# Performance work log

Hardware: AMD Instinct MI355X
Metric: run time of the kernel (lower is better)

The kernel has to match this reference:

```python
import jax, jax.numpy as jnp
import numpy as np

NG, NT, E = 2500, 20000, 640000
SRC_DIM, DST_DIM, HID, OUT, NCLS = 128, 500, 128, 128, 16


def setup_inputs() -> dict:
    key = jax.random.key(0)
    ks = jax.random.split(key, 11)
    d = {
        "gene_feats": jax.random.normal(ks[0], (NG, SRC_DIM), jnp.float32),
        "train_feats": jax.random.normal(ks[1], (NT, DST_DIM), jnp.float32),
        "edge_src": jax.random.randint(ks[2], (E,), 0, NG),
        "edge_dst": jax.random.randint(ks[3], (E,), 0, NT),
        # conv1: SAGEConv((src_dim, dst_dim) -> hidden)
        "W1_neigh": jax.random.normal(ks[4], (SRC_DIM, HID), jnp.float32) / np.sqrt(SRC_DIM),
        "W1_self": jax.random.normal(ks[5], (DST_DIM, HID), jnp.float32) / np.sqrt(DST_DIM),
        "b1": jnp.zeros((HID,), jnp.float32),
        # conv2: SAGEConv(hidden -> out); src input is the raw gene features
        "W2_neigh": jax.random.normal(ks[6], (HID, OUT), jnp.float32) / np.sqrt(HID),
        "W2_self": jax.random.normal(ks[7], (HID, OUT), jnp.float32) / np.sqrt(HID),
        "b2": jnp.zeros((OUT,), jnp.float32),
        # classifier MLP
        "Wc1": jax.random.normal(ks[8], (OUT, OUT), jnp.float32) / np.sqrt(OUT),
        "bc1": jnp.zeros((OUT,), jnp.float32),
        "Wc2": jax.random.normal(ks[9], (OUT, NCLS), jnp.float32) / np.sqrt(OUT),
        "bc2": jnp.zeros((NCLS,), jnp.float32),
    }
    return d


def _segment_mean(msgs, dst, num_segments):
    # mean over in-edges; isolated dst nodes get 0 (DGL convention)
    sums = jax.ops.segment_sum(msgs, dst, num_segments=num_segments)
    cnt = jax.ops.segment_sum(jnp.ones((msgs.shape[0],), msgs.dtype), dst,
                              num_segments=num_segments)
    return sums / jnp.maximum(cnt, 1.0)[:, None]


def reference(gene_feats, train_feats, edge_src, edge_dst,
              W1_neigh, W1_self, b1, W2_neigh, W2_self, b2,
              Wc1, bc1, Wc2, bc2):
    # mean-aggregate gene (src) features onto train (dst) nodes
    agg = _segment_mean(gene_feats[edge_src], edge_dst, NT)  # [NT, SRC_DIM]
    # conv1: fc_self(h_dst) + fc_neigh(mean_neigh) + bias, then ReLU
    h1 = jax.nn.relu(train_feats @ W1_self + agg @ W1_neigh + b1)  # [NT, HID]
    # conv2 reuses raw gene features as src -> same mean aggregation
    h2 = jax.nn.relu(h1 @ W2_self + agg @ W2_neigh + b2)  # [NT, OUT]
    # classifier: Linear -> ReLU -> Linear
    return jax.nn.relu(h2 @ Wc1 + bc1) @ Wc2 + bc2  # [NT, NCLS]
```

## Files before the change

### kernel.cpp

```cpp
#include <hip/hip_runtime.h>


#define NG 2500
#define NT 20000
#define NE 640000
#define NCLS 16
#define CAP 96
#define BCAP 1536
#define NBIN 625

typedef unsigned short u16;
typedef unsigned int u32;

typedef float f32x4 __attribute__((ext_vector_type(4)));
typedef __bf16 bf16x8 __attribute__((ext_vector_type(8)));

__device__ __forceinline__ float b2f(u16 u) { return __uint_as_float(((u32)u) << 16); }
__device__ __forceinline__ float blo(u32 p) { return __uint_as_float(p << 16); }
__device__ __forceinline__ float bhi(u32 p) { return __uint_as_float(p & 0xffff0000u); }
__device__ __forceinline__ u16 f2b(float f) {
    u32 u = __float_as_uint(f);
    return (u16)((u + 0x7fffu + ((u >> 16) & 1u)) >> 16);
}

#define B1N 81920
#define B2N 32768
#define B3N 16384
#define B4N 2048
#define NEB 625
#define GNB 625
#define PKB 520

__global__ __launch_bounds__(256) void k_prep(
    const int* __restrict__ edst,
    u32* __restrict__ hist,
    const float* __restrict__ gene, u32* __restrict__ GH32,
    const float* __restrict__ W1n, const float* __restrict__ W1s,
    const float* __restrict__ W2n, const float* __restrict__ W2s,
    const float* __restrict__ Wc1, const float* __restrict__ Wc2,
    u16* __restrict__ B1h, u16* __restrict__ B1l,
    u16* __restrict__ B2h, u16* __restrict__ B2l,
    u16* __restrict__ B3h, u16* __restrict__ B3l,
    u16* __restrict__ B4h, u16* __restrict__ B4l) {
    int blk = blockIdx.x, t = threadIdx.x;
    if (blk < NEB) {
        __shared__ u32 lh[NBIN];
        for (int i = t; i < NBIN; i += 256) lh[i] = 0;
        __syncthreads();
        int e0 = (blk * 256 + t) * 4;
        const int4 d4 = *(const int4*)(edst + e0);
        int dd[4] = {d4.x, d4.y, d4.z, d4.w};
#pragma unroll
        for (int i = 0; i < 4; ++i) {
            unsigned d = (unsigned)dd[i];
            if (d < NT) atomicAdd(&lh[d >> 5], 1u);
        }
        __syncthreads();
        for (int i = t; i < NBIN; i += 256)
            hist[(size_t)blk * NBIN + i] = lh[i];
        return;
    }
    if (blk < NEB + GNB) {
        int idx = (blk - NEB) * 256 + t;
        float2 v = ((const float2*)gene)[idx];
        GH32[idx] = (u32)f2b(v.x) | ((u32)f2b(v.y) << 16);
        return;
    }
    int idx = (blk - NEB - GNB) * 256 + t;
    float v = 0.f;
    u16 *ph = 0, *pl = 0;
    int off = 0;
    if (idx < B1N) {
        int j = idx & 7, l = (idx >> 3) & 63, rest = idx >> 9;
        int g = rest & 7, kk = rest >> 3;
        int k = kk * 32 + ((l >> 4) << 3) + j, n = (g << 4) + (l & 15);
        if (k < 500) v = W1s[k * 128 + n];
        else if (k >= 512) v = W1n[(k - 512) * 128 + n];
        ph = B1h; pl = B1l; off = idx;
    } else if (idx < B1N + B2N) {
        int e = idx - B1N;
        int j = e & 7, l = (e >> 3) & 63, rest = e >> 9;
        int g = rest & 7, kk = rest >> 3;
        int k = kk * 32 + ((l >> 4) << 3) + j, n = (g << 4) + (l & 15);
        v = (k < 128) ? W2s[k * 128 + n] : W2n[(k - 128) * 128 + n];
        ph = B2h; pl = B2l; off = e;
    } else if (idx < B1N + B2N + B3N) {
        int e = idx - (B1N + B2N);
        int j = e & 7, l = (e >> 3) & 63, rest = e >> 9;
        int g = rest & 7, kk = rest >> 3;
        int k = kk * 32 + ((l >> 4) << 3) + j, n = (g << 4) + (l & 15);
        v = Wc1[k * 128 + n];
        ph = B3h; pl = B3l; off = e;
    } else if (idx < B1N + B2N + B3N + B4N) {
        int e = idx - (B1N + B2N + B3N);
        int j = e & 7, l = (e >> 3) & 63, kk = e >> 9;
        int k = kk * 32 + ((l >> 4) << 3) + j, n = l & 15;
        v = Wc2[k * 16 + n];
        ph = B4h; pl = B4l; off = e;
    }
    if (ph) {
        u16 hi = f2b(v);
        u16 lo = f2b(v - b2f(hi));
        ph[off] = hi;
        pl[off] = lo;
    }
}

__global__ __launch_bounds__(256) void k_scan(
    const u32* __restrict__ hist, u32* __restrict__ boff,
    int* __restrict__ bcnt) {
    int bin = blockIdx.x, t = threadIdx.x;
    __shared__ u32 part[256];
    u32 s0 = 0, s1 = 0, s2 = 0;
    int i0 = 3 * t;
    if (i0 < NBIN) s0 = hist[(size_t)i0 * NBIN + bin];
    if (i0 + 1 < NBIN) s1 = hist[(size_t)(i0 + 1) * NBIN + bin];
    if (i0 + 2 < NBIN) s2 = hist[(size_t)(i0 + 2) * NBIN + bin];
    u32 mine = s0 + s1 + s2;
    part[t] = mine;
    __syncthreads();
    for (int off = 1; off < 256; off <<= 1) {
        u32 x = (t >= off) ? part[t - off] : 0u;
        __syncthreads();
        part[t] += x;
        __syncthreads();
    }
    u32 base = part[t] - mine;
    if (i0 < NBIN) boff[(size_t)bin * NBIN + i0] = base;
    if (i0 + 1 < NBIN) boff[(size_t)bin * NBIN + i0 + 1] = base + s0;
    if (i0 + 2 < NBIN) boff[(size_t)bin * NBIN + i0 + 2] = base + s0 + s1;
    if (t == 255) bcnt[bin] = (int)part[255];
}

__global__ __launch_bounds__(256) void k_scat(
    const int* __restrict__ esrc, const int* __restrict__ edst,
    const u32* __restrict__ boff, u32* __restrict__ bkt) {
    int blk = blockIdx.x, t = threadIdx.x;
    __shared__ u32 lcur[NBIN];
    for (int i = t; i < NBIN; i += 256) lcur[i] = 0;
    __syncthreads();
    int e0 = (blk * 256 + t) * 4;
    const int4 s4 = *(const int4*)(esrc + e0);
    const int4 d4 = *(const int4*)(edst + e0);
    int ss[4] = {s4.x, s4.y, s4.z, s4.w};
    int dd[4] = {d4.x, d4.y, d4.z, d4.w};
#pragma unroll
    for (int i = 0; i < 4; ++i) {
        unsigned d = (unsigned)dd[i];
        if (d < NT) {
            int bin = (int)(d >> 5);
            u32 rank = atomicAdd(&lcur[bin], 1u);
            u32 pos = boff[(size_t)bin * NBIN + blk] + rank;
            if (pos < BCAP)
                bkt[(size_t)bin * BCAP + pos] = ((d & 31u) << 16) | (u32)ss[i];
        }
    }
}

__global__ __launch_bounds__(256, 8) void k_agg(
    const int* __restrict__ bcnt, const u32* __restrict__ bkt,
    const u16* __restrict__ GH,
    u32* __restrict__ AGH, u32* __restrict__ AGL) {
    __shared__ __align__(16) u16 SRT[16 * CAP];
    __shared__ int POS[16];
    int t = threadIdx.x;
    int bk = blockIdx.x >> 1, half = blockIdx.x & 1;

    if (t < 16) POS[t] = 0;
    int bc = bcnt[bk];
    if (bc > BCAP) bc = BCAP;
    __syncthreads();

    int rlo = half * 16;
    for (int i = t; i < bc; i += 256) {
        u32 e = bkt[(size_t)bk * BCAP + i];
        int r = (int)(e >> 16) - rlo;
        if ((unsigned)r < 16u) {
            int p = atomicAdd(&POS[r], 1);
            if (p < CAP) SRT[r * CAP + p] = (u16)(e & 0xffffu);
        }
    }
    __syncthreads();

    int gr = t >> 4, cg = t & 15;
    int ctrue = POS[gr];
    int c = ctrue > CAP ? CAP : ctrue;
    const u16* crow = SRT + gr * CAP;
    int nfull = c >> 3;
    uint4 i40 = *(const uint4*)(crow);
    uint4 i41 = *(const uint4*)(crow + 8);
    uint4 i42 = *(const uint4*)(crow + 16);
    uint4 i43 = *(const uint4*)(crow + 24);
    float a[8];
#pragma unroll
    for (int p = 0; p < 8; ++p) a[p] = 0.f;

#define ACC(p)                                      \
    do {                                            \
        a[0] += blo((p).x); a[1] += bhi((p).x);     \
        a[2] += blo((p).y); a[3] += bhi((p).y);     \
        a[4] += blo((p).z); a[5] += bhi((p).z);     \
        a[6] += blo((p).w); a[7] += bhi((p).w);     \
    } while (0)
    auto GHLoad = [&](int s) -> uint4 {
        return *(const uint4*)(GH + (size_t)s * 128 + cg * 8);
    };
    auto batch8 = [&](uint4 iq) {
        uint4 P0 = GHLoad((int)(iq.x & 0xffffu));
        uint4 P1 = GHLoad((int)(iq.x >> 16));
        uint4 P2 = GHLoad((int)(iq.y & 0xffffu));
        uint4 P3 = GHLoad((int)(iq.y >> 16));
        uint4 P4 = GHLoad((int)(iq.z & 0xffffu));
        uint4 P5 = GHLoad((int)(iq.z >> 16));
        uint4 P6 = GHLoad((int)(iq.w & 0xffffu));
        uint4 P7 = GHLoad((int)(iq.w >> 16));
        ACC(P0); ACC(P1); ACC(P2); ACC(P3);
        ACC(P4); ACC(P5); ACC(P6); ACC(P7);
    };

    if (nfull > 0) batch8(i40);
    if (nfull > 1) batch8(i41);
    if (nfull > 2) batch8(i42);
    if (nfull > 3) batch8(i43);
    for (int b = 4; b < nfull; ++b) batch8(*(const uint4*)(crow + b * 8));
    {
        int j = nfull * 8;
        if (j < c) {
            uint4 i4 = *(const uint4*)(crow + j);
            u32 w[4] = {i4.x, i4.y, i4.z, i4.w};
#pragma unroll
            for (int k = 0; k < 8; ++k) {
                int s = (int)((w[k >> 1] >> ((k & 1) * 16)) & 0xffffu);
                bool live = (j + k) < c;
                s = live ? s : 0;
                uint4 p = GHLoad(s);
                if (live) ACC(p);
            }
        }
    }
#undef ACC

    float inv = (ctrue > 0) ? 1.f / (float)ctrue : 0.f;
    size_t base = (size_t)(blockIdx.x * 16 + gr) * 64 + cg * 4;
#pragma unroll
    for (int p = 0; p < 4; ++p) {
        float x = a[2 * p] * inv, y = a[2 * p + 1] * inv;
        u16 hx = f2b(x), hy = f2b(y);
        AGH[base + p] = (u32)hx | ((u32)hy << 16);
        AGL[base + p] = (u32)f2b(x - b2f(hx)) | ((u32)f2b(y - b2f(hy)) << 16);
    }
}

__global__ __launch_bounds__(512, 4) void k_mlp(
    const u32* __restrict__ AGH, const u32* __restrict__ AGL,
    const float* __restrict__ train,
    const u16* __restrict__ B1h, const u16* __restrict__ B1l,
    const u16* __restrict__ B2h, const u16* __restrict__ B2l,
    const u16* __restrict__ B3h, const u16* __restrict__ B3l,
    const u16* __restrict__ B4h, const u16* __restrict__ B4l,
    const float* __restrict__ b1, const float* __restrict__ b2,
    const float* __restrict__ bc1, const float* __restrict__ bc2,
    float* __restrict__ out) {
    __shared__ __align__(16) u16 SMEM[26112];
    u16* SAGh = SMEM;
    u16* SAGl = SMEM + 4352;
    u16* S1h = SMEM + 8704;
    u16* S1l = SMEM + 13056;
    u16* S2h = SMEM + 17408;
    u16* S2l = SMEM + 21760;
    u16* TS = SMEM + 8704;

    int t = threadIdx.x;
    int row0 = blockIdx.x * 32;

    float4 st[8];
    {
        const float4* tb = (const float4*)(train + (size_t)row0 * 500);
#pragma unroll
        for (int i = 0; i < 7; ++i) st[i] = tb[t + i * 512];
        if (t < 416) st[7] = tb[t + 3584];
    }
    uint4 ah4 = ((const uint4*)AGH)[(size_t)row0 * 16 + t];
    uint4 al4 = ((const uint4*)AGL)[(size_t)row0 * 16 + t];

    {
        u32* T32 = (u32*)TS;
#pragma unroll
        for (int i = 0; i < 8; ++i) {
            int idx = t + i * 512;
            if (i == 7 && t >= 416) break;
            int r = idx / 125, c4 = idx - r * 125;
            int base = r * 260 + c4 * 2;
            T32[base] = (u32)f2b(st[i].x) | ((u32)f2b(st[i].y) << 16);
            T32[base + 1] = (u32)f2b(st[i].z) | ((u32)f2b(st[i].w) << 16);
        }
        if (t < 192) {
            int r = t / 6, c4 = t - r * 6;
            T32[r * 260 + 250 + c4] = 0;
        }
    }
    {
        int r = t >> 4, c16 = t & 15;
        int base = r * 68 + c16 * 4;
        u32* SH = (u32*)SAGh;
        u32* SL = (u32*)SAGl;
        SH[base] = ah4.x; SH[base + 1] = ah4.y;
        SH[base + 2] = ah4.z; SH[base + 3] = ah4.w;
        SL[base] = al4.x; SL[base + 1] = al4.y;
        SL[base + 2] = al4.z; SL[base + 3] = al4.w;
    }
    __syncthreads();

    int lane = t & 63, g = t >> 6;
    int m = lane & 15, q = lane >> 4, n16 = lane & 15;

    int hr0 = m * 136 + q * 8;
    int hr1 = (16 + m) * 136 + q * 8;
    int cr0 = q * 4, cr1 = 16 + q * 4;
    const f32x4 z4 = {0.f, 0.f, 0.f, 0.f};
    f32x4 acc0 = z4, acc1 = z4;
    const u16* tA0 = TS + m * 520 + q * 8;
    const u16* tA1 = TS + (16 + m) * 520 + q * 8;

#pragma unroll
    for (int kk = 0; kk < 16; ++kk) {
        bf16x8 a0 = *(const bf16x8*)(tA0 + kk * 32);
        bf16x8 a1 = *(const bf16x8*)(tA1 + kk * 32);
        size_t bo = ((size_t)(kk * 8 + g) * 64 + lane) * 8;
        bf16x8 bh = *(const bf16x8*)(B1h + bo);
        bf16x8 bl = *(const bf16x8*)(B1l + bo);
        acc0 = __builtin_amdgcn_mfma_f32_16x16x32_bf16(a0, bh, acc0, 0, 0, 0);
        acc0 = __builtin_amdgcn_mfma_f32_16x16x32_bf16(a0, bl, acc0, 0, 0, 0);
        acc1 = __builtin_amdgcn_mfma_f32_16x16x32_bf16(a1, bh, acc1, 0, 0, 0);
        acc1 = __builtin_amdgcn_mfma_f32_16x16x32_bf16(a1, bl, acc1, 0, 0, 0);
    }
#pragma unroll
    for (int kk = 16; kk < 20; ++kk) {
        int o = (kk - 16) * 32;
        bf16x8 ah0 = *(const bf16x8*)(SAGh + hr0 + o);
        bf16x8 al0 = *(const bf16x8*)(SAGl + hr0 + o);
        bf16x8 ah1 = *(const bf16x8*)(SAGh + hr1 + o);
        bf16x8 al1 = *(const bf16x8*)(SAGl + hr1 + o);
        size_t bo = ((size_t)(kk * 8 + g) * 64 + lane) * 8;
        bf16x8 bh = *(const bf16x8*)(B1h + bo);
        bf16x8 bl = *(const bf16x8*)(B1l + bo);
        acc0 = __builtin_amdgcn_mfma_f32_16x16x32_bf16(ah0, bh, acc0, 0, 0, 0);
        acc0 = __builtin_amdgcn_mfma_f32_16x16x32_bf16(ah0, bl, acc0, 0, 0, 0);
        acc0 = __builtin_amdgcn_mfma_f32_16x16x32_bf16(al0, bh, acc0, 0, 0, 0);
        acc1 = __builtin_amdgcn_mfma_f32_16x16x32_bf16(ah1, bh, acc1, 0, 0, 0);
        acc1 = __builtin_amdgcn_mfma_f32_16x16x32_bf16(ah1, bl, acc1, 0, 0, 0);
        acc1 = __builtin_amdgcn_mfma_f32_16x16x32_bf16(al1, bh, acc1, 0, 0, 0);
    }
    __syncthreads();
    {
        int n = g * 16 + n16;
        float bias = b1[n];
#pragma unroll
        for (int rg = 0; rg < 4; ++rg) {
            float v0 = acc0[rg] + bias; v0 = v0 > 0.f ? v0 : 0.f;
            float v1 = acc1[rg] + bias; v1 = v1 > 0.f ? v1 : 0.f;
            u16 h0 = f2b(v0), h1v = f2b(v1);
            S1h[(cr0 + rg) * 136 + n] = h0; S1l[(cr0 + rg) * 136 + n] = f2b(v0 - b2f(h0));
            S1h[(cr1 + rg) * 136 + n] = h1v; S1l[(cr1 + rg) * 136 + n] = f2b(v1 - b2f(h1v));
        }
    }
    __syncthreads();

    acc0 = z4; acc1 = z4;
#pragma unroll
    for (int kk = 0; kk < 8; ++kk) {
        const u16* Ph = (kk < 4) ? S1h : SAGh;
        const u16* Pl = (kk < 4) ? S1l : SAGl;
        int o = (kk & 3) * 32;
        bf16x8 ah0 = *(const bf16x8*)(Ph + hr0 + o);
        bf16x8 al0 = *(const bf16x8*)(Pl + hr0 + o);
        bf16x8 ah1 = *(const bf16x8*)(Ph + hr1 + o);
        bf16x8 al1 = *(const bf16x8*)(Pl + hr1 + o);
        size_t bo = ((size_t)(kk * 8 + g) * 64 + lane) * 8;
        bf16x8 bh = *(const bf16x8*)(B2h + bo);
        bf16x8 bl = *(const bf16x8*)(B2l + bo);
        acc0 = __builtin_amdgcn_mfma_f32_16x16x32_bf16(ah0, bh, acc0, 0, 0, 0);
        acc0 = __builtin_amdgcn_mfma_f32_16x16x32_bf16(ah0, bl, acc0, 0, 0, 0);
        acc0 = __builtin_amdgcn_mfma_f32_16x16x32_bf16(al0, bh, acc0, 0, 0, 0);
        acc1 = __builtin_amdgcn_mfma_f32_16x16x32_bf16(ah1, bh, acc1, 0, 0, 0);
        acc1 = __builtin_amdgcn_mfma_f32_16x16x32_bf16(ah1, bl, acc1, 0, 0, 0);
        acc1 = __builtin_amdgcn_mfma_f32_16x16x32_bf16(al1, bh, acc1, 0, 0, 0);
    }
    {
        int n = g * 16 + n16;
        float bias = b2[n];
#pragma unroll
        for (int rg = 0; rg < 4; ++rg) {
            float v0 = acc0[rg] + bias; v0 = v0 > 0.f ? v0 : 0.f;
            float v1 = acc1[rg] + bias; v1 = v1 > 0.f ? v1 : 0.f;
            u16 h0 = f2b(v0), h1v = f2b(v1);
            S2h[(cr0 + rg) * 136 + n] = h0; S2l[(cr0 + rg) * 136 + n] = f2b(v0 - b2f(h0));
            S2h[(cr1 + rg) * 136 + n] = h1v; S2l[(cr1 + rg) * 136 + n] = f2b(v1 - b2f(h1v));
        }
    }
    __syncthreads();

    acc0 = z4; acc1 = z4;
#pragma unroll
    for (int kk = 0; kk < 4; ++kk) {
        int o = kk * 32;
        bf16x8 ah0 = *(const bf16x8*)(S2h + hr0 + o);
        bf16x8 al0 = *(const bf16x8*)(S2l + hr0 + o);
        bf16x8 ah1 = *(const bf16x8*)(S2h + hr1 + o);
        bf16x8 al1 = *(const bf16x8*)(S2l + hr1 + o);
        size_t bo = ((size_t)(kk * 8 + g) * 64 + lane) * 8;
        bf16x8 bh = *(const bf16x8*)(B3h + bo);
        bf16x8 bl = *(const bf16x8*)(B3l + bo);
        acc0 = __builtin_amdgcn_mfma_f32_16x16x32_bf16(ah0, bh, acc0, 0, 0, 0);
        acc0 = __builtin_amdgcn_mfma_f32_16x16x32_bf16(ah0, bl, acc0, 0, 0, 0);
        acc0 = __builtin_amdgcn_mfma_f32_16x16x32_bf16(al0, bh, acc0, 0, 0, 0);
        acc1 = __builtin_amdgcn_mfma_f32_16x16x32_bf16(ah1, bh, acc1, 0, 0, 0);
        acc1 = __builtin_amdgcn_mfma_f32_16x16x32_bf16(ah1, bl, acc1, 0, 0, 0);
        acc1 = __builtin_amdgcn_mfma_f32_16x16x32_bf16(al1, bh, acc1, 0, 0, 0);
    }
    {
        int n = g * 16 + n16;
        float bias = bc1[n];
#pragma unroll
        for (int rg = 0; rg < 4; ++rg) {
            float v0 = acc0[rg] + bias; v0 = v0 > 0.f ? v0 : 0.f;
            float v1 = acc1[rg] + bias; v1 = v1 > 0.f ? v1 : 0.f;
            u16 h0 = f2b(v0), h1v = f2b(v1);
            S1h[(cr0 + rg) * 136 + n] = h0; S1l[(cr0 + rg) * 136 + n] = f2b(v0 - b2f(h0));
            S1h[(cr1 + rg) * 136 + n] = h1v; S1l[(cr1 + rg) * 136 + n] = f2b(v1 - b2f(h1v));
        }
    }
    __syncthreads();

    if (g < 2) {
        int hr = (g == 0) ? hr0 : hr1;
        int cr = (g == 0) ? cr0 : cr1;
        f32x4 a4 = z4;
#pragma unroll
        for (int kk = 0; kk < 4; ++kk) {
            bf16x8 ah = *(const bf16x8*)(S1h + hr + kk * 32);
            bf16x8 al = *(const bf16x8*)(S1l + hr + kk * 32);
            size_t bo = ((size_t)kk * 64 + lane) * 8;
            bf16x8 bh = *(const bf16x8*)(B4h + bo);
            bf16x8 bl = *(const bf16x8*)(B4l + bo);
            a4 = __builtin_amdgcn_mfma_f32_16x16x32_bf16(ah, bh, a4, 0, 0, 0);
            a4 = __builtin_amdgcn_mfma_f32_16x16x32_bf16(ah, bl, a4, 0, 0, 0);
            a4 = __builtin_amdgcn_mfma_f32_16x16x32_bf16(al, bh, a4, 0, 0, 0);
        }
        float bias = bc2[n16];
#pragma unroll
        for (int rg = 0; rg < 4; ++rg)
            out[(size_t)(row0 + cr + rg) * NCLS + n16] = a4[rg] + bias;
    }
}

extern "C" void kernel_launch(void* const* d_in, const int* in_sizes, int n_in,
                              void* d_out, int out_size, void* d_ws, size_t ws_size,
                              hipStream_t stream) {
    const float* gene = (const float*)d_in[0];
    const float* train = (const float*)d_in[1];
    const int* esrc = (const int*)d_in[2];
    const int* edst = (const int*)d_in[3];

    char* ws = (char*)d_ws;
    int* bcnt = (int*)(ws + 0);
    u32* hist = (u32*)(ws + 4096);
    u32* boff = (u32*)(ws + 1566720);
    u32* bkt = (u32*)(ws + 3129344);
    u16* GH = (u16*)(ws + 6969344);
    u32* AGH = (u32*)(ws + 7609344);
    u32* AGL = (u32*)(ws + 12729344);
    u16* B1h = (u16*)(ws + 17849344);
    u16* B1l = (u16*)(ws + 18013184);
    u16* B2h = (u16*)(ws + 18177024);
    u16* B2l = (u16*)(ws + 18242560);
    u16* B3h = (u16*)(ws + 18308096);
    u16* B3l = (u16*)(ws + 18340864);
    u16* B4h = (u16*)(ws + 18373632);
    u16* B4l = (u16*)(ws + 18377728);

    k_prep<<<NEB + GNB + PKB, 256, 0, stream>>>(
        edst, hist, gene, (u32*)GH,
        (const float*)d_in[4], (const float*)d_in[5], (const float*)d_in[7],
        (const float*)d_in[8], (const float*)d_in[10], (const float*)d_in[12],
        B1h, B1l, B2h, B2l, B3h, B3l, B4h, B4l);
    k_scan<<<NBIN, 256, 0, stream>>>(hist, boff, bcnt);
    k_scat<<<NEB, 256, 0, stream>>>(esrc, edst, boff, bkt);
    k_agg<<<NT / 16, 256, 0, stream>>>(bcnt, bkt, GH, AGH, AGL);
    k_mlp<<<NT / 32, 512, 0, stream>>>(
        AGH, AGL, train, B1h, B1l, B2h, B2l, B3h, B3l, B4h, B4l,
        (const float*)d_in[6], (const float*)d_in[9], (const float*)d_in[11],
        (const float*)d_in[13], (float*)d_out);
}
```

Measured before the change: 153.8 us.

## Fuse prep, scan, scatter and aggregation into one cooperative kernel with grid syncs

```diff
diff --git a/kernel.cpp b/kernel.cpp
--- a/kernel.cpp
+++ b/kernel.cpp
@@ -1,4 +1,7 @@
 #include <hip/hip_runtime.h>
+#include <hip/hip_cooperative_groups.h>
+
+namespace cg = cooperative_groups;
 
 
 #define NG 2500
@@ -30,43 +33,13 @@
 #define NEB 625
 #define GNB 625
 #define PKB 520
-
-__global__ __launch_bounds__(256) void k_prep(
-    const int* __restrict__ edst,
-    u32* __restrict__ hist,
-    const float* __restrict__ gene, u32* __restrict__ GH32,
-    const float* __restrict__ W1n, const float* __restrict__ W1s,
-    const float* __restrict__ W2n, const float* __restrict__ W2s,
-    const float* __restrict__ Wc1, const float* __restrict__ Wc2,
-    u16* __restrict__ B1h, u16* __restrict__ B1l,
-    u16* __restrict__ B2h, u16* __restrict__ B2l,
-    u16* __restrict__ B3h, u16* __restrict__ B3l,
-    u16* __restrict__ B4h, u16* __restrict__ B4l) {
-    int blk = blockIdx.x, t = threadIdx.x;
-    if (blk < NEB) {
-        __shared__ u32 lh[NBIN];
-        for (int i = t; i < NBIN; i += 256) lh[i] = 0;
-        __syncthreads();
-        int e0 = (blk * 256 + t) * 4;
-        const int4 d4 = *(const int4*)(edst + e0);
-        int dd[4] = {d4.x, d4.y, d4.z, d4.w};
-#pragma unroll
-        for (int i = 0; i < 4; ++i) {
-            unsigned d = (unsigned)dd[i];
-            if (d < NT) atomicAdd(&lh[d >> 5], 1u);
-        }
-        __syncthreads();
-        for (int i = t; i < NBIN; i += 256)
-            hist[(size_t)blk * NBIN + i] = lh[i];
-        return;
-    }
-    if (blk < NEB + GNB) {
-        int idx = (blk - NEB) * 256 + t;
-        float2 v = ((const float2*)gene)[idx];
-        GH32[idx] = (u32)f2b(v.x) | ((u32)f2b(v.y) << 16);
-        return;
-    }
-    int idx = (blk - NEB - GNB) * 256 + t;
+#define NCB (NEB + GNB + PKB)
+
+__device__ __forceinline__ void pack_one(
+    int idx, const float* W1n, const float* W1s, const float* W2n,
+    const float* W2s, const float* Wc1, const float* Wc2,
+    u16* B1h, u16* B1l, u16* B2h, u16* B2l, u16* B3h, u16* B3l,
+    u16* B4h, u16* B4l) {
     float v = 0.f;
     u16 *ph = 0, *pl = 0;
     int off = 0;
@@ -106,66 +79,10 @@
     }
 }
 
-__global__ __launch_bounds__(256) void k_scan(
-    const u32* __restrict__ hist, u32* __restrict__ boff,
-    int* __restrict__ bcnt) {
-    int bin = blockIdx.x, t = threadIdx.x;
-    __shared__ u32 part[256];
-    u32 s0 = 0, s1 = 0, s2 = 0;
-    int i0 = 3 * t;
-    if (i0 < NBIN) s0 = hist[(size_t)i0 * NBIN + bin];
-    if (i0 + 1 < NBIN) s1 = hist[(size_t)(i0 + 1) * NBIN + bin];
-    if (i0 + 2 < NBIN) s2 = hist[(size_t)(i0 + 2) * NBIN + bin];
-    u32 mine = s0 + s1 + s2;
-    part[t] = mine;
-    __syncthreads();
-    for (int off = 1; off < 256; off <<= 1) {
-        u32 x = (t >= off) ? part[t - off] : 0u;
-        __syncthreads();
-        part[t] += x;
-        __syncthreads();
-    }
-    u32 base = part[t] - mine;
-    if (i0 < NBIN) boff[(size_t)bin * NBIN + i0] = base;
-    if (i0 + 1 < NBIN) boff[(size_t)bin * NBIN + i0 + 1] = base + s0;
-    if (i0 + 2 < NBIN) boff[(size_t)bin * NBIN + i0 + 2] = base + s0 + s1;
-    if (t == 255) bcnt[bin] = (int)part[255];
-}
-
-__global__ __launch_bounds__(256) void k_scat(
-    const int* __restrict__ esrc, const int* __restrict__ edst,
-    const u32* __restrict__ boff, u32* __restrict__ bkt) {
-    int blk = blockIdx.x, t = threadIdx.x;
-    __shared__ u32 lcur[NBIN];
-    for (int i = t; i < NBIN; i += 256) lcur[i] = 0;
-    __syncthreads();
-    int e0 = (blk * 256 + t) * 4;
-    const int4 s4 = *(const int4*)(esrc + e0);
-    const int4 d4 = *(const int4*)(edst + e0);
-    int ss[4] = {s4.x, s4.y, s4.z, s4.w};
-    int dd[4] = {d4.x, d4.y, d4.z, d4.w};
-#pragma unroll
-    for (int i = 0; i < 4; ++i) {
-        unsigned d = (unsigned)dd[i];
-        if (d < NT) {
-            int bin = (int)(d >> 5);
-            u32 rank = atomicAdd(&lcur[bin], 1u);
-            u32 pos = boff[(size_t)bin * NBIN + blk] + rank;
-            if (pos < BCAP)
-                bkt[(size_t)bin * BCAP + pos] = ((d & 31u) << 16) | (u32)ss[i];
-        }
-    }
-}
-
-__global__ __launch_bounds__(256, 8) void k_agg(
-    const int* __restrict__ bcnt, const u32* __restrict__ bkt,
-    const u16* __restrict__ GH,
-    u32* __restrict__ AGH, u32* __restrict__ AGL) {
-    __shared__ __align__(16) u16 SRT[16 * CAP];
-    __shared__ int POS[16];
-    int t = threadIdx.x;
-    int bk = blockIdx.x >> 1, half = blockIdx.x & 1;
-
+__device__ __forceinline__ void agg_body(
+    int blk16, const int* bcnt, const u32* bkt, const u16* GH,
+    u32* AGH, u32* AGL, u16* SRT, int* POS, int t) {
+    int bk = blk16 >> 1, half = blk16 & 1;
     if (t < 16) POS[t] = 0;
     int bc = bcnt[bk];
     if (bc > BCAP) bc = BCAP;
@@ -182,7 +99,7 @@
     }
     __syncthreads();
 
-    int gr = t >> 4, cg = t & 15;
+    int gr = t >> 4, cg16 = t & 15;
     int ctrue = POS[gr];
     int c = ctrue > CAP ? CAP : ctrue;
     const u16* crow = SRT + gr * CAP;
@@ -203,7 +120,7 @@
         a[6] += blo((p).w); a[7] += bhi((p).w);     \
     } while (0)
     auto GHLoad = [&](int s) -> uint4 {
-        return *(const uint4*)(GH + (size_t)s * 128 + cg * 8);
+        return *(const uint4*)(GH + (size_t)s * 128 + cg16 * 8);
     };
     auto batch8 = [&](uint4 iq) {
         uint4 P0 = GHLoad((int)(iq.x & 0xffffu));
@@ -241,7 +158,7 @@
 #undef ACC
 
     float inv = (ctrue > 0) ? 1.f / (float)ctrue : 0.f;
-    size_t base = (size_t)(blockIdx.x * 16 + gr) * 64 + cg * 4;
+    size_t base = (size_t)(blk16 * 16 + gr) * 64 + cg16 * 4;
 #pragma unroll
     for (int p = 0; p < 4; ++p) {
         float x = a[2 * p] * inv, y = a[2 * p + 1] * inv;
@@ -249,6 +166,205 @@
         AGH[base + p] = (u32)hx | ((u32)hy << 16);
         AGL[base + p] = (u32)f2b(x - b2f(hx)) | ((u32)f2b(y - b2f(hy)) << 16);
     }
+}
+
+__global__ __launch_bounds__(256, 8) void k_coop(
+    const int* __restrict__ esrc, const int* __restrict__ edst,
+    u32* __restrict__ hist, u32* __restrict__ boff, int* __restrict__ bcnt,
+    u32* __restrict__ bkt,
+    const float* __restrict__ gene, u32* __restrict__ GH32,
+    const u16* __restrict__ GH,
+    u32* __restrict__ AGH, u32* __restrict__ AGL,
+    const float* __restrict__ W1n, const float* __restrict__ W1s,
+    const float* __restrict__ W2n, const float* __restrict__ W2s,
+    const float* __restrict__ Wc1, const float* __restrict__ Wc2,
+    u16* __restrict__ B1h, u16* __restrict__ B1l,
+    u16* __restrict__ B2h, u16* __restrict__ B2l,
+    u16* __restrict__ B3h, u16* __restrict__ B3l,
+    u16* __restrict__ B4h, u16* __restrict__ B4l) {
+    __shared__ __align__(16) u32 UN[800];
+    u32* lh = UN;
+    u32* part = UN;
+    u32* lcur = UN;
+    u16* SRT = (u16*)UN;
+    int* POS = (int*)(UN + 768);
+
+    cg::grid_group grid = cg::this_grid();
+    int blk = blockIdx.x, t = threadIdx.x;
+
+    int4 s4 = {0, 0, 0, 0}, d4 = {0, 0, 0, 0};
+
+    if (blk < NEB) {
+        for (int i = t; i < NBIN; i += 256) lh[i] = 0;
+        __syncthreads();
+        int e0 = (blk * 256 + t) * 4;
+        s4 = *(const int4*)(esrc + e0);
+        d4 = *(const int4*)(edst + e0);
+        int dd[4] = {d4.x, d4.y, d4.z, d4.w};
+#pragma unroll
+        for (int i = 0; i < 4; ++i) {
+            unsigned d = (unsigned)dd[i];
+            if (d < NT) atomicAdd(&lh[d >> 5], 1u);
+        }
+        __syncthreads();
+        for (int i = t; i < NBIN; i += 256)
+            hist[(size_t)blk * NBIN + i] = lh[i];
+    } else if (blk < NEB + GNB) {
+        int idx = (blk - NEB) * 256 + t;
+        float2 v = ((const float2*)gene)[idx];
+        GH32[idx] = (u32)f2b(v.x) | ((u32)f2b(v.y) << 16);
+    } else {
+        int idx = (blk - NEB - GNB) * 256 + t;
+        pack_one(idx, W1n, W1s, W2n, W2s, Wc1, Wc2,
+                 B1h, B1l, B2h, B2l, B3h, B3l, B4h, B4l);
+    }
+    grid.sync();
+
+    if (blk < NBIN) {
+        int bin = blk;
+        u32 s0 = 0, s1 = 0, s2 = 0;
+        int i0 = 3 * t;
+        if (i0 < NBIN) s0 = hist[(size_t)i0 * NBIN + bin];
+        if (i0 + 1 < NBIN) s1 = hist[(size_t)(i0 + 1) * NBIN + bin];
+        if (i0 + 2 < NBIN) s2 = hist[(size_t)(i0 + 2) * NBIN + bin];
+        u32 mine = s0 + s1 + s2;
+        part[t] = mine;
+        __syncthreads();
+        for (int off = 1; off < 256; off <<= 1) {
+            u32 x = (t >= off) ? part[t - off] : 0u;
+            __syncthreads();
+            part[t] += x;
+            __syncthreads();
+        }
+        u32 base = part[t] - mine;
+        if (i0 < NBIN) boff[(size_t)bin * NBIN + i0] = base;
+        if (i0 + 1 < NBIN) boff[(size_t)bin * NBIN + i0 + 1] = base + s0;
+        if (i0 + 2 < NBIN) boff[(size_t)bin * NBIN + i0 + 2] = base + s0 + s1;
+        if (t == 255) bcnt[bin] = (int)part[255];
+    }
+    grid.sync();
+
+    if (blk < NEB) {
+        for (int i = t; i < NBIN; i += 256) lcur[i] = 0;
+        __syncthreads();
+        int ss[4] = {s4.x, s4.y, s4.z, s4.w};
+        int dd[4] = {d4.x, d4.y, d4.z, d4.w};
+#pragma unroll
+        for (int i = 0; i < 4; ++i) {
+            unsigned d = (unsigned)dd[i];
+            if (d < NT) {
+                int bin = (int)(d >> 5);
+                u32 rank = atomicAdd(&lcur[bin], 1u);
+                u32 pos = boff[(size_t)bin * NBIN + blk] + rank;
+                if (pos < BCAP)
+                    bkt[(size_t)bin * BCAP + pos] =
+                        ((d & 31u) << 16) | (u32)ss[i];
+            }
+        }
+    }
+    grid.sync();
+
+    if (blk < NT / 16)
+        agg_body(blk, bcnt, bkt, GH, AGH, AGL, SRT, POS, t);
+}
+
+__global__ __launch_bounds__(256) void k_prep(
+    const int* __restrict__ edst,
+    u32* __restrict__ hist,
+    const float* __restrict__ gene, u32* __restrict__ GH32,
+    const float* __restrict__ W1n, const float* __restrict__ W1s,
+    const float* __restrict__ W2n, const float* __restrict__ W2s,
+    const float* __restrict__ Wc1, const float* __restrict__ Wc2,
+    u16* __restrict__ B1h, u16* __restrict__ B1l,
+    u16* __restrict__ B2h, u16* __restrict__ B2l,
+    u16* __restrict__ B3h, u16* __restrict__ B3l,
+    u16* __restrict__ B4h, u16* __restrict__ B4l) {
+    int blk = blockIdx.x, t = threadIdx.x;
+    if (blk < NEB) {
+        __shared__ u32 lh[NBIN];
+        for (int i = t; i < NBIN; i += 256) lh[i] = 0;
+        __syncthreads();
+        int e0 = (blk * 256 + t) * 4;
+        const int4 d4 = *(const int4*)(edst + e0);
+        int dd[4] = {d4.x, d4.y, d4.z, d4.w};
+#pragma unroll
+        for (int i = 0; i < 4; ++i) {
+            unsigned d = (unsigned)dd[i];
+            if (d < NT) atomicAdd(&lh[d >> 5], 1u);
+        }
+        __syncthreads();
+        for (int i = t; i < NBIN; i += 256)
+            hist[(size_t)blk * NBIN + i] = lh[i];
+        return;
+    }
+    if (blk < NEB + GNB) {
+        int idx = (blk - NEB) * 256 + t;
+        float2 v = ((const float2*)gene)[idx];
+        GH32[idx] = (u32)f2b(v.x) | ((u32)f2b(v.y) << 16);
+        return;
+    }
+    pack_one((blk - NEB - GNB) * 256 + t, W1n, W1s, W2n, W2s, Wc1, Wc2,
+             B1h, B1l, B2h, B2l, B3h, B3l, B4h, B4l);
+}
+
+__global__ __launch_bounds__(256) void k_scan(
+    const u32* __restrict__ hist, u32* __restrict__ boff,
+    int* __restrict__ bcnt) {
+    int bin = blockIdx.x, t = threadIdx.x;
+    __shared__ u32 part[256];
+    u32 s0 = 0, s1 = 0, s2 = 0;
+    int i0 = 3 * t;
+    if (i0 < NBIN) s0 = hist[(size_t)i0 * NBIN + bin];
+    if (i0 + 1 < NBIN) s1 = hist[(size_t)(i0 + 1) * NBIN + bin];
+    if (i0 + 2 < NBIN) s2 = hist[(size_t)(i0 + 2) * NBIN + bin];
+    u32 mine = s0 + s1 + s2;
+    part[t] = mine;
+    __syncthreads();
+    for (int off = 1; off < 256; off <<= 1) {
+        u32 x = (t >= off) ? part[t - off] : 0u;
+        __syncthreads();
+        part[t] += x;
+        __syncthreads();
+    }
+    u32 base = part[t] - mine;
+    if (i0 < NBIN) boff[(size_t)bin * NBIN + i0] = base;
+    if (i0 + 1 < NBIN) boff[(size_t)bin * NBIN + i0 + 1] = base + s0;
+    if (i0 + 2 < NBIN) boff[(size_t)bin * NBIN + i0 + 2] = base + s0 + s1;
+    if (t == 255) bcnt[bin] = (int)part[255];
+}
+
+__global__ __launch_bounds__(256) void k_scat(
+    const int* __restrict__ esrc, const int* __restrict__ edst,
+    const u32* __restrict__ boff, u32* __restrict__ bkt) {
+    int blk = blockIdx.x, t = threadIdx.x;
+    __shared__ u32 lcur[NBIN];
+    for (int i = t; i < NBIN; i += 256) lcur[i] = 0;
+    __syncthreads();
+    int e0 = (blk * 256 + t) * 4;
+    const int4 s4 = *(const int4*)(esrc + e0);
+    const int4 d4 = *(const int4*)(edst + e0);
+    int ss[4] = {s4.x, s4.y, s4.z, s4.w};
+    int dd[4] = {d4.x, d4.y, d4.z, d4.w};
+#pragma unroll
+    for (int i = 0; i < 4; ++i) {
+        unsigned d = (unsigned)dd[i];
+        if (d < NT) {
+            int bin = (int)(d >> 5);
+            u32 rank = atomicAdd(&lcur[bin], 1u);
+            u32 pos = boff[(size_t)bin * NBIN + blk] + rank;
+            if (pos < BCAP)
+                bkt[(size_t)bin * BCAP + pos] = ((d & 31u) << 16) | (u32)ss[i];
+        }
+    }
+}
+
+__global__ __launch_bounds__(256, 8) void k_agg(
+    const int* __restrict__ bcnt, const u32* __restrict__ bkt,
+    const u16* __restrict__ GH,
+    u32* __restrict__ AGH, u32* __restrict__ AGL) {
+    __shared__ __align__(16) u16 SRT[16 * CAP];
+    __shared__ int POS[16];
+    agg_body(blockIdx.x, bcnt, bkt, GH, AGH, AGL, SRT, POS, threadIdx.x);
 }
 
 __global__ __launch_bounds__(512, 4) void k_mlp(
@@ -479,14 +595,37 @@
     u16* B4h = (u16*)(ws + 18373632);
     u16* B4l = (u16*)(ws + 18377728);
 
-    k_prep<<<NEB + GNB + PKB, 256, 0, stream>>>(
-        edst, hist, gene, (u32*)GH,
-        (const float*)d_in[4], (const float*)d_in[5], (const float*)d_in[7],
-        (const float*)d_in[8], (const float*)d_in[10], (const float*)d_in[12],
-        B1h, B1l, B2h, B2l, B3h, B3l, B4h, B4l);
-    k_scan<<<NBIN, 256, 0, stream>>>(hist, boff, bcnt);
-    k_scat<<<NEB, 256, 0, stream>>>(esrc, edst, boff, bkt);
-    k_agg<<<NT / 16, 256, 0, stream>>>(bcnt, bkt, GH, AGH, AGL);
+    u32* GH32 = (u32*)GH;
+    const float* W1n = (const float*)d_in[4];
+    const float* W1s = (const float*)d_in[5];
+    const float* W2n = (const float*)d_in[7];
+    const float* W2s = (const float*)d_in[8];
+    const float* Wc1 = (const float*)d_in[10];
+    const float* Wc2 = (const float*)d_in[12];
+    const u16* GHc = (const u16*)GH;
+
+    static int use_coop = 1;
+    if (use_coop) {
+        void* args[] = {
+            (void*)&esrc, (void*)&edst, (void*)&hist, (void*)&boff,
+            (void*)&bcnt, (void*)&bkt, (void*)&gene, (void*)&GH32,
+            (void*)&GHc, (void*)&AGH, (void*)&AGL,
+            (void*)&W1n, (void*)&W1s, (void*)&W2n, (void*)&W2s,
+            (void*)&Wc1, (void*)&Wc2,
+            (void*)&B1h, (void*)&B1l, (void*)&B2h, (void*)&B2l,
+            (void*)&B3h, (void*)&B3l, (void*)&B4h, (void*)&B4l};
+        hipError_t err = hipLaunchCooperativeKernel(
+            (const void*)k_coop, dim3(NCB), dim3(256), args, 0, stream);
+        if (err != hipSuccess) use_coop = 0;
+    }
+    if (!use_coop) {
+        k_prep<<<NEB + GNB + PKB, 256, 0, stream>>>(
+            edst, hist, gene, GH32, W1n, W1s, W2n, W2s, Wc1, Wc2,
+            B1h, B1l, B2h, B2l, B3h, B3l, B4h, B4l);
+        k_scan<<<NBIN, 256, 0, stream>>>(hist, boff, bcnt);
+        k_scat<<<NEB, 256, 0, stream>>>(esrc, edst, boff, bkt);
+        k_agg<<<NT / 16, 256, 0, stream>>>(bcnt, bkt, GHc, AGH, AGL);
+    }
     k_mlp<<<NT / 32, 512, 0, stream>>>(
         AGH, AGL, train, B1h, B1l, B2h, B2l, B3h, B3l, B4h, B4l,
         (const float*)d_in[6], (const float*)d_in[9], (const float*)d_in[11],
```

After: 154.0 us. Within noise of the previous version (+0.2%).
